# Kernel optimization log

Hardware: AMD Instinct MI355X
Metric: run time of the kernel (lower is better)

The kernel has to match this reference:

```python
import jax, jax.numpy as jnp
import numpy as np

# Model dims
H = 1024          # hidden_size
I = 2048          # intermediate_size
E = 8             # num_experts
IE = I // E       # expert_intermediate_size = 256
V = 100000        # vocab_size
B, S = 8, 2048


def _rowwise_quantize(x):
    """Dynamic per-row int8 quantization (faithful to dynamic_quantize_int8, per_channel=True).
    Returns quantized values kept in float32 (identical values to int8->float cast) and per-row scale."""
    max_vals = jnp.max(jnp.abs(x), axis=-1, keepdims=True)
    scale = jnp.maximum(max_vals / 127.0, 1e-8)
    x_q = jnp.clip(jnp.round(x / scale), -128.0, 127.0)
    return x_q, scale[..., 0]


def _quantize_weight(w):
    """Per-output-channel int8 quantization of a [K, N] weight (as in from_float)."""
    max_vals = jnp.max(jnp.abs(w), axis=0, keepdims=True)      # [1, N]
    scale = jnp.maximum(max_vals / 127.0, 1e-8)
    w_q = jnp.clip(jnp.round(w / scale), -128.0, 127.0).astype(jnp.int8)
    return w_q, scale[0]


def setup_inputs() -> dict:
    key = jax.random.key(0)
    ks = jax.random.split(key, 6)
    hidden_states = jax.random.normal(ks[0], (B, S, H), dtype=jnp.float32)
    token_ids = jax.random.randint(ks[1], (B, S), 0, V, dtype=jnp.int32)

    # Pre-quantized expert weights (int8) with per-output-channel fp32 scales.
    gate_w = jax.random.normal(ks[2], (E, H, IE), dtype=jnp.float32) * 0.02
    up_w = jax.random.normal(ks[3], (E, H, IE), dtype=jnp.float32) * 0.02
    down_w = jax.random.normal(ks[4], (E, IE, H), dtype=jnp.float32) * 0.02
    gate_q, gate_scale = jax.vmap(_quantize_weight)(gate_w)   # [E,H,IE] int8, [E,IE]
    up_q, up_scale = jax.vmap(_quantize_weight)(up_w)         # [E,H,IE] int8, [E,IE]
    down_q, down_scale = jax.vmap(_quantize_weight)(down_w)   # [E,IE,H] int8, [E,H]

    # Deterministic contiguous token->expert mapping (V divisible by E here).
    token_to_expert = jnp.minimum(jnp.arange(V, dtype=jnp.int32) // (V // E), E - 1)

    return {
        "hidden_states": hidden_states,
        "token_ids": token_ids,
        "gate_q": gate_q, "gate_scale": gate_scale,
        "up_q": up_q, "up_scale": up_scale,
        "down_q": down_q, "down_scale": down_scale,
        "token_to_expert": token_to_expert,
    }


def reference(hidden_states, token_ids, gate_q, gate_scale, up_q, up_scale,
              down_q, down_scale, token_to_expert):
    Bh, Sh, Hh = hidden_states.shape
    n_exp = gate_q.shape[0]
    vocab = token_to_expert.shape[0]

    tid = jnp.clip(token_ids, 0, vocab - 1)
    expert_ids = token_to_expert[tid].reshape(-1)             # [T]

    x = hidden_states.reshape(-1, Hh)                          # [T, H]
    # Per-row activation quantization is expert-independent -> do it once for all tokens.
    x_q, x_s = _rowwise_quantize(x)                            # [T,H], [T]

    gq = gate_q.astype(jnp.float32)
    uq = up_q.astype(jnp.float32)
    dq = down_q.astype(jnp.float32)

    out = jnp.zeros_like(x)
    for e in range(n_exp):  # small fixed expert count
        # fused quantize-GEMM: int8 matmul + per-row activation scale + per-col weight scale
        gate = (x_q @ gq[e]) * x_s[:, None] * gate_scale[e][None, :]   # [T, IE]
        up = (x_q @ uq[e]) * x_s[:, None] * up_scale[e][None, :]       # [T, IE]
        inter = jax.nn.silu(gate) * up
        i_q, i_s = _rowwise_quantize(inter)
        o = (i_q @ dq[e]) * i_s[:, None] * down_scale[e][None, :]      # [T, H]
        out = jnp.where((expert_ids == e)[:, None], o, out)
    return out.reshape(Bh, Sh, Hh)
```

## Files before the change

### kernel.cpp

```cpp
#include <hip/hip_runtime.h>

typedef int   int4v   __attribute__((ext_vector_type(4)));
typedef float float4v __attribute__((ext_vector_type(4)));

#define T_TOK 16384
#define HD    1024
#define IE    256
#define EN    8
#define VSZ   100000

#define M_OFF 16
#define M_TS1 25

#define XQ_OFF   0ull
#define PB1_OFF  21053440ull
#define PB2_OFF  25247744ull
#define PERM_OFF 27344896ull
#define XS_OFF   27410688ull
#define META_OFF 27542272ull
#define BC_OFF   27542528ull
#define BB_OFF   27544576ull

__device__ __forceinline__ void gload16(const void* g, void* l) {
    __builtin_amdgcn_global_load_lds(
        (const __attribute__((address_space(1))) unsigned int*)g,
        (__attribute__((address_space(3))) unsigned int*)l,
        16, 0, 0);
}

__global__ void k_hist(const int* __restrict__ ids, const int* __restrict__ t2e,
                       int* __restrict__ bc) {
    __shared__ int h[EN];
    if (threadIdx.x < EN) h[threadIdx.x] = 0;
    __syncthreads();
    int t = blockIdx.x * 256 + threadIdx.x;
    int id = ids[t]; id = min(max(id, 0), VSZ - 1);
    atomicAdd(&h[t2e[id]], 1);
    __syncthreads();
    if (threadIdx.x < EN) bc[blockIdx.x * EN + threadIdx.x] = h[threadIdx.x];
}

__global__ __launch_bounds__(512) void k_scan(const int* __restrict__ bc,
                                              int* __restrict__ bbase,
                                              int* __restrict__ meta) {
    int e = threadIdx.x >> 6;
    int b = threadIdx.x & 63;
    int c = bc[b * EN + e];
    int inc = c;
    #pragma unroll
    for (int s = 1; s < 64; s <<= 1) {
        int v = __shfl_up(inc, s, 64);
        if (b >= s) inc += v;
    }
    int exc = inc - c;
    __shared__ int tot[EN];
    __shared__ int goff[EN];
    if (b == 63) tot[e] = inc;
    __syncthreads();
    if (threadIdx.x == 0) {
        int off = 0, t1 = 0;
        meta[M_OFF] = 0; meta[M_TS1] = 0;
        #pragma unroll
        for (int i = 0; i < EN; ++i) {
            goff[i] = off;
            int cc = tot[i];
            off += cc; t1 += (cc + 31) >> 5;
            meta[M_OFF + i + 1] = off;
            meta[M_TS1 + i + 1] = t1;
        }
    }
    __syncthreads();
    bbase[b * EN + e] = goff[e] + exc;
}

__global__ void k_assign(const int* __restrict__ ids, const int* __restrict__ t2e,
                         const int* __restrict__ bbase, int* __restrict__ perm) {
    __shared__ int cur[EN];
    if (threadIdx.x < EN) cur[threadIdx.x] = bbase[blockIdx.x * EN + threadIdx.x];
    __syncthreads();
    int t = blockIdx.x * 256 + threadIdx.x;
    int id = ids[t]; id = min(max(id, 0), VSZ - 1);
    int e = t2e[id];
    int slot = atomicAdd(&cur[e], 1);
    perm[slot] = t;
}

__global__ __launch_bounds__(256) void k_pre(const float* __restrict__ hidden,
                                             const int* __restrict__ gq,
                                             const int* __restrict__ uq,
                                             const int* __restrict__ dq,
                                             signed char* __restrict__ xq,
                                             float* __restrict__ xs,
                                             signed char* __restrict__ pb1,
                                             signed char* __restrict__ pb2) {
    int b = blockIdx.x;
    if (b < 4096) {
        int w = threadIdx.x >> 6, lane = threadIdx.x & 63;
        int token = (b << 2) + w;
        const float* row = hidden + (size_t)token * HD;
        float v[16];
        #pragma unroll
        for (int j = 0; j < 4; ++j) {
            float4v f = *(const float4v*)(row + lane * 16 + j * 4);
            v[j*4+0] = f[0]; v[j*4+1] = f[1]; v[j*4+2] = f[2]; v[j*4+3] = f[3];
        }
        float mx = 0.0f;
        #pragma unroll
        for (int j = 0; j < 16; ++j) mx = fmaxf(mx, fabsf(v[j]));
        #pragma unroll
        for (int s = 1; s < 64; s <<= 1) mx = fmaxf(mx, __shfl_xor(mx, s, 64));
        float sc = fmaxf(mx / 127.0f, 1e-8f);
        if (lane == 0) xs[token] = sc;
        int4v pk;
        #pragma unroll
        for (int j = 0; j < 4; ++j) {
            int bb[4];
            #pragma unroll
            for (int u = 0; u < 4; ++u) {
                float t = rintf(v[j*4+u] / sc);
                t = fminf(fmaxf(t, -128.0f), 127.0f);
                bb[u] = (int)t;
            }
            pk[j] = (bb[0] & 255) | ((bb[1] & 255) << 8) | ((bb[2] & 255) << 16) | (bb[3] << 24);
        }
        *(int4v*)(xq + (size_t)token * HD + lane * 16) = pk;
    } else {
        int idx = (b - 4096) * 256 + threadIdx.x;
        if (idx < 262144) {
            int n = idx & 511, kc = (idx >> 9) & 63, e = idx >> 15;
            const int* src = (n < 256) ? gq + (((size_t)((e << 10) + (kc << 4)) << 8) + n)
                                       : uq + (((size_t)((e << 10) + (kc << 4)) << 8) + (n - 256));
            int4v pk;
            #pragma unroll
            for (int jj = 0; jj < 4; ++jj) {
                int b0 = src[(size_t)(jj * 4 + 0) << 8], b1 = src[(size_t)(jj * 4 + 1) << 8];
                int b2 = src[(size_t)(jj * 4 + 2) << 8], b3 = src[(size_t)(jj * 4 + 3) << 8];
                pk[jj] = (b0 & 255) | ((b1 & 255) << 8) | ((b2 & 255) << 16) | (b3 << 24);
            }
            *(int4v*)(pb1 + ((size_t)((((e << 6) + kc) << 9) + n) << 4)) = pk;
        } else {
            int j = idx - 262144;
            int n = j & 1023, kc = (j >> 10) & 15, e = j >> 14;
            const int* src = dq + (((size_t)((e << 8) + (kc << 4)) << 10) + n);
            int4v pk;
            #pragma unroll
            for (int jj = 0; jj < 4; ++jj) {
                int b0 = src[(size_t)(jj * 4 + 0) << 10], b1 = src[(size_t)(jj * 4 + 1) << 10];
                int b2 = src[(size_t)(jj * 4 + 2) << 10], b3 = src[(size_t)(jj * 4 + 3) << 10];
                pk[jj] = (b0 & 255) | ((b1 & 255) << 8) | ((b2 & 255) << 16) | (b3 << 24);
            }
            *(int4v*)(pb2 + ((size_t)((((e << 4) + kc) << 10) + n) << 4)) = pk;
        }
    }
}

__global__ __launch_bounds__(256, 2) void k_mlp(const signed char* __restrict__ xq,
                                                const signed char* __restrict__ pb1,
                                                const signed char* __restrict__ pb2,
                                                const float* __restrict__ xs,
                                                const float* __restrict__ gsc,
                                                const float* __restrict__ usc,
                                                const float* __restrict__ dsc,
                                                const int* __restrict__ meta,
                                                const int* __restrict__ perm,
                                                float* __restrict__ out) {
    int b = (blockIdx.x & 7) * 65 + (blockIdx.x >> 3);
    int e = -1, m0 = 0, gend = 0;
    #pragma unroll
    for (int i = 0; i < EN; ++i) {
        int s0 = meta[M_TS1 + i], s1 = meta[M_TS1 + i + 1];
        if (b >= s0 && b < s1) { e = i; m0 = meta[M_OFF + i] + ((b - s0) << 5); gend = meta[M_OFF + i + 1]; }
    }
    if (e < 0) return;
    const int w = threadIdx.x >> 6, lane = threadIdx.x & 63;
    const int q = lane >> 4, r = lane & 15;

    __shared__ __align__(16) signed char lB[2][32768];
    __shared__ __align__(16) signed char arena[8192];
    float* pmax = (float*)(arena + 4096);
    float* rsc  = (float*)(arena + 4608);
    int*   ptok = (int*)(arena + 4736);

    if (threadIdx.x < 32) ptok[threadIdx.x] = perm[min(m0 + (int)threadIdx.x, T_TOK - 1)];
    __syncthreads();

    int tokr[2][4];
    #pragma unroll
    for (int mi = 0; mi < 2; ++mi)
        #pragma unroll
        for (int g = 0; g < 4; ++g)
            tokr[mi][g] = ptok[(mi << 4) + (q << 2) + g];

    const signed char* pbe1 = pb1 + (size_t)e * (64 * 512 * 16);
    const signed char* pbe2 = pb2 + (size_t)e * (16 * 1024 * 16);
    const int arow = (w << 4) + (lane >> 2);
    const int acq  = (lane & 3) ^ ((lane >> 2) & 3);
    const signed char* ga_base = xq + (size_t)ptok[arow & 31] * HD + (acq << 4);

    #define G1_STAGE(buf, kt)                                                          \
        {                                                                              \
            int kc0 = (kt) << 2;                                                       \
            _Pragma("unroll")                                                          \
            for (int j = 0; j < 8; ++j) {                                              \
                int n = ((j << 6) + lane) ^ ((w & 1) << 3);                            \
                gload16(pbe1 + (((size_t)(kc0 + w) * 512 + n) << 4),                   \
                        &lB[buf][((w << 3) + j) << 10]);                               \
            }                                                                          \
            if (w < 2) gload16(ga_base + ((kt) << 6), arena + ((buf) << 11) + (w << 10)); \
        }

    #define G2_STAGE(buf, st)                                                          \
        {                                                                              \
            int kc0 = ((st) & 3) << 2; int nhs = (st) >> 2;                            \
            _Pragma("unroll")                                                          \
            for (int j = 0; j < 8; ++j) {                                              \
                int n = ((j << 6) + lane) ^ ((w & 1) << 3);                            \
                gload16(pbe2 + (((size_t)(kc0 + w) * 1024 + (nhs << 9) + n) << 4),     \
                        &lB[buf][((w << 3) + j) << 10]);                               \
            }                                                                          \
        }

    int4v zero = {0, 0, 0, 0};
    int4v accg[2][4], accu[2][4];
    #pragma unroll
    for (int mi = 0; mi < 2; ++mi)
        #pragma unroll
        for (int i = 0; i < 4; ++i) { accg[mi][i] = zero; accu[mi][i] = zero; }

    G1_STAGE(0, 0);
    for (int kt = 0; kt < 16; ++kt) {
        int cur = kt & 1;
        __syncthreads();
        if (kt < 15) G1_STAGE(cur ^ 1, kt + 1);
        int4v a[2];
        #pragma unroll
        for (int mi = 0; mi < 2; ++mi)
            a[mi] = *(const int4v*)&arena[(cur << 11) + ((((mi << 4) + r) << 6) + ((q ^ (r & 3)) << 4))];
        #pragma unroll
        for (int i = 0; i < 4; ++i) {
            int n = (w << 6) + (i << 4) + r;
            int sg = (q << 9) + (n ^ ((q & 1) << 3));
            int su = (q << 9) + ((n + 256) ^ ((q & 1) << 3));
            int4v bg = *(const int4v*)&lB[cur][sg << 4];
            int4v bu = *(const int4v*)&lB[cur][su << 4];
            #pragma unroll
            for (int mi = 0; mi < 2; ++mi) {
                accg[mi][i] = __builtin_amdgcn_mfma_i32_16x16x64_i8(a[mi], bg, accg[mi][i], 0, 0, 0);
                accu[mi][i] = __builtin_amdgcn_mfma_i32_16x16x64_i8(a[mi], bu, accu[mi][i], 0, 0, 0);
            }
        }
    }
    #undef G1_STAGE

    G2_STAGE(0, 0);

    float gs[4], us[4];
    #pragma unroll
    for (int i = 0; i < 4; ++i) {
        int n = (w << 6) + (i << 4) + r;
        gs[i] = gsc[e * IE + n];
        us[i] = usc[e * IE + n];
    }
    float xsr[2][4];
    #pragma unroll
    for (int mi = 0; mi < 2; ++mi)
        #pragma unroll
        for (int g = 0; g < 4; ++g)
            xsr[mi][g] = xs[tokr[mi][g]];

    float inter[2][4][4];
    float pm[2][4];
    #pragma unroll
    for (int mi = 0; mi < 2; ++mi)
        #pragma unroll
        for (int g = 0; g < 4; ++g) {
            float mx = 0.0f;
            #pragma unroll
            for (int i = 0; i < 4; ++i) {
                float gv = (float)accg[mi][i][g] * xsr[mi][g] * gs[i];
                float uv = (float)accu[mi][i][g] * xsr[mi][g] * us[i];
                float sg = gv / (1.0f + expf(-gv));
                float vv = sg * uv;
                inter[mi][i][g] = vv;
                mx = fmaxf(mx, fabsf(vv));
            }
            #pragma unroll
            for (int s = 1; s < 16; s <<= 1) mx = fmaxf(mx, __shfl_xor(mx, s, 64));
            pm[mi][g] = mx;
        }

    __syncthreads();
    if (r == 0) {
        #pragma unroll
        for (int mi = 0; mi < 2; ++mi)
            #pragma unroll
            for (int g = 0; g < 4; ++g)
                pmax[(w << 5) + (mi << 4) + (q << 2) + g] = pm[mi][g];
    }
    __syncthreads();
    if (threadIdx.x < 32) {
        int row = threadIdx.x;
        float mx = fmaxf(fmaxf(pmax[row], pmax[32 + row]), fmaxf(pmax[64 + row], pmax[96 + row]));
        rsc[row] = fmaxf(mx / 127.0f, 1e-8f);
    }
    __syncthreads();
    float rscr[2][4];
    #pragma unroll
    for (int mi = 0; mi < 2; ++mi)
        #pragma unroll
        for (int g = 0; g < 4; ++g)
            rscr[mi][g] = rsc[(mi << 4) + (q << 2) + g];
    __syncthreads();

    #pragma unroll
    for (int mi = 0; mi < 2; ++mi)
        #pragma unroll
        for (int g = 0; g < 4; ++g) {
            int row = (mi << 4) + (q << 2) + g;
            float sc = rscr[mi][g];
            #pragma unroll
            for (int i = 0; i < 4; ++i) {
                float t = rintf(inter[mi][i][g] / sc);
                t = fminf(fmaxf(t, -128.0f), 127.0f);
                arena[(row << 8) + ((((w << 2) + i) ^ (row & 3)) << 4) + r] = (signed char)(int)t;
            }
        }

    int4v acc2[2][8];
    for (int st = 0; st < 8; ++st) {
        int cur = st & 1;
        __syncthreads();
        if (st < 7) G2_STAGE(cur ^ 1, st + 1);
        if ((st & 3) == 0) {
            #pragma unroll
            for (int mi = 0; mi < 2; ++mi)
                #pragma unroll
                for (int i = 0; i < 8; ++i) acc2[mi][i] = zero;
        }
        int4v a2[2];
        #pragma unroll
        for (int mi = 0; mi < 2; ++mi) {
            int row2 = (mi << 4) + r;
            a2[mi] = *(const int4v*)&arena[(row2 << 8) + (((((st & 3) << 2) + q) ^ (r & 3)) << 4)];
        }
        #pragma unroll
        for (int i = 0; i < 8; ++i) {
            int n = (w << 7) + (i << 4) + r;
            int sb = (q << 9) + (n ^ ((q & 1) << 3));
            int4v bb = *(const int4v*)&lB[cur][sb << 4];
            #pragma unroll
            for (int mi = 0; mi < 2; ++mi)
                acc2[mi][i] = __builtin_amdgcn_mfma_i32_16x16x64_i8(a2[mi], bb, acc2[mi][i], 0, 0, 0);
        }
        if ((st & 3) == 3) {
            int nhs = st >> 2;
            float ds[8];
            #pragma unroll
            for (int i = 0; i < 8; ++i)
                ds[i] = dsc[e * HD + (nhs << 9) + (w << 7) + (i << 4) + r];
            #pragma unroll
            for (int mi = 0; mi < 2; ++mi)
                #pragma unroll
                for (int g = 0; g < 4; ++g) {
                    int slot = m0 + (mi << 4) + (q << 2) + g;
                    if (slot < gend) {
                        size_t ob = (size_t)tokr[mi][g] * HD + (nhs << 9) + (w << 7) + r;
                        #pragma unroll
                        for (int i = 0; i < 8; ++i)
                            out[ob + (i << 4)] = (float)acc2[mi][i][g] * rscr[mi][g] * ds[i];
                    }
                }
        }
    }
    #undef G2_STAGE
}

extern "C" void kernel_launch(void* const* d_in, const int* in_sizes, int n_in,
                              void* d_out, int out_size, void* d_ws, size_t ws_size,
                              hipStream_t stream) {
    const float* hidden = (const float*)d_in[0];
    const int*   ids    = (const int*)d_in[1];
    const int*   gq     = (const int*)d_in[2];
    const float* gsc    = (const float*)d_in[3];
    const int*   uq     = (const int*)d_in[4];
    const float* usc    = (const float*)d_in[5];
    const int*   dq     = (const int*)d_in[6];
    const float* dsc    = (const float*)d_in[7];
    const int*   t2e    = (const int*)d_in[8];
    float* out = (float*)d_out;

    char* ws = (char*)d_ws;
    signed char* xq  = (signed char*)(ws + XQ_OFF);
    signed char* pb1 = (signed char*)(ws + PB1_OFF);
    signed char* pb2 = (signed char*)(ws + PB2_OFF);
    int*   perm = (int*)(ws + PERM_OFF);
    float* xs   = (float*)(ws + XS_OFF);
    int*   meta = (int*)(ws + META_OFF);
    int*   bc   = (int*)(ws + BC_OFF);
    int*   bbase= (int*)(ws + BB_OFF);

    k_hist<<<64, 256, 0, stream>>>(ids, t2e, bc);
    k_scan<<<1, 512, 0, stream>>>(bc, bbase, meta);
    k_assign<<<64, 256, 0, stream>>>(ids, t2e, bbase, perm);
    k_pre<<<5632, 256, 0, stream>>>(hidden, gq, uq, dq, xq, xs, pb1, pb2);
    k_mlp<<<520, 256, 0, stream>>>(xq, pb1, pb2, xs, gsc, usc, dsc, meta, perm, out);
}
```

Before: 204.6 us.

## Double M tile to 64 tokens and triple-buffer LDS with cross-phase prefetch

```diff
diff --git a/kernel.cpp b/kernel.cpp
--- a/kernel.cpp
+++ b/kernel.cpp
@@ -28,6 +28,12 @@
         16, 0, 0);
 }
 
+#define LDS_BAR() do { \
+    asm volatile("s_waitcnt lgkmcnt(0)" ::: "memory"); \
+    __builtin_amdgcn_s_barrier(); \
+    __builtin_amdgcn_sched_barrier(0); \
+} while (0)
+
 __global__ void k_hist(const int* __restrict__ ids, const int* __restrict__ t2e,
                        int* __restrict__ bc) {
     __shared__ int h[EN];
@@ -64,7 +70,7 @@
         for (int i = 0; i < EN; ++i) {
             goff[i] = off;
             int cc = tot[i];
-            off += cc; t1 += (cc + 31) >> 5;
+            off += cc; t1 += (cc + 63) >> 6;
             meta[M_OFF + i + 1] = off;
             meta[M_TS1 + i + 1] = t1;
         }
@@ -154,7 +160,7 @@
     }
 }
 
-__global__ __launch_bounds__(256, 2) void k_mlp(const signed char* __restrict__ xq,
+__global__ __launch_bounds__(256, 1) void k_mlp(const signed char* __restrict__ xq,
                                                 const signed char* __restrict__ pb1,
                                                 const signed char* __restrict__ pb2,
                                                 const float* __restrict__ xs,
@@ -164,29 +170,29 @@
                                                 const int* __restrict__ meta,
                                                 const int* __restrict__ perm,
                                                 float* __restrict__ out) {
-    int b = (blockIdx.x & 7) * 65 + (blockIdx.x >> 3);
+    int b = (blockIdx.x & 7) * 33 + (blockIdx.x >> 3);
     int e = -1, m0 = 0, gend = 0;
     #pragma unroll
     for (int i = 0; i < EN; ++i) {
         int s0 = meta[M_TS1 + i], s1 = meta[M_TS1 + i + 1];
-        if (b >= s0 && b < s1) { e = i; m0 = meta[M_OFF + i] + ((b - s0) << 5); gend = meta[M_OFF + i + 1]; }
+        if (b >= s0 && b < s1) { e = i; m0 = meta[M_OFF + i] + ((b - s0) << 6); gend = meta[M_OFF + i + 1]; }
     }
     if (e < 0) return;
     const int w = threadIdx.x >> 6, lane = threadIdx.x & 63;
     const int q = lane >> 4, r = lane & 15;
 
-    __shared__ __align__(16) signed char lB[2][32768];
-    __shared__ __align__(16) signed char arena[8192];
-    float* pmax = (float*)(arena + 4096);
-    float* rsc  = (float*)(arena + 4608);
-    int*   ptok = (int*)(arena + 4736);
-
-    if (threadIdx.x < 32) ptok[threadIdx.x] = perm[min(m0 + (int)threadIdx.x, T_TOK - 1)];
-    __syncthreads();
-
-    int tokr[2][4];
-    #pragma unroll
-    for (int mi = 0; mi < 2; ++mi)
+    __shared__ __align__(16) signed char lB[3][32768];
+    __shared__ __align__(16) signed char arena[16384];
+    float* pmax = (float*)(arena + 12288);
+    float* rsc  = (float*)(arena + 13312);
+    int*   ptok = (int*)(arena + 13568);
+
+    if (threadIdx.x < 64) ptok[threadIdx.x] = perm[min(m0 + (int)threadIdx.x, T_TOK - 1)];
+    __syncthreads();
+
+    int tokr[4][4];
+    #pragma unroll
+    for (int mi = 0; mi < 4; ++mi)
         #pragma unroll
         for (int g = 0; g < 4; ++g)
             tokr[mi][g] = ptok[(mi << 4) + (q << 2) + g];
@@ -195,7 +201,27 @@
     const signed char* pbe2 = pb2 + (size_t)e * (16 * 1024 * 16);
     const int arow = (w << 4) + (lane >> 2);
     const int acq  = (lane & 3) ^ ((lane >> 2) & 3);
-    const signed char* ga_base = xq + (size_t)ptok[arow & 31] * HD + (acq << 4);
+    const signed char* ga_base = xq + (size_t)ptok[arow] * HD + (acq << 4);
+
+    float gs[4], us[4];
+    #pragma unroll
+    for (int i = 0; i < 4; ++i) {
+        int n = (w << 6) + (i << 4) + r;
+        gs[i] = gsc[e * IE + n];
+        us[i] = usc[e * IE + n];
+    }
+    float xsr[4][4];
+    #pragma unroll
+    for (int mi = 0; mi < 4; ++mi)
+        #pragma unroll
+        for (int g = 0; g < 4; ++g)
+            xsr[mi][g] = xs[tokr[mi][g]];
+    float ds16[2][8];
+    #pragma unroll
+    for (int nh = 0; nh < 2; ++nh)
+        #pragma unroll
+        for (int i = 0; i < 8; ++i)
+            ds16[nh][i] = dsc[e * HD + (nh << 9) + (w << 7) + (i << 4) + r];
 
     #define G1_STAGE(buf, kt)                                                          \
         {                                                                              \
@@ -206,12 +232,12 @@
                 gload16(pbe1 + (((size_t)(kc0 + w) * 512 + n) << 4),                   \
                         &lB[buf][((w << 3) + j) << 10]);                               \
             }                                                                          \
-            if (w < 2) gload16(ga_base + ((kt) << 6), arena + ((buf) << 11) + (w << 10)); \
-        }
-
-    #define G2_STAGE(buf, st)                                                          \
+            gload16(ga_base + ((kt) << 6), arena + ((buf) << 12) + (w << 10));         \
+        }
+
+    #define G2_STAGE(buf, st2)                                                         \
         {                                                                              \
-            int kc0 = ((st) & 3) << 2; int nhs = (st) >> 2;                            \
+            int kc0 = ((st2) & 3) << 2; int nhs = (st2) >> 2;                          \
             _Pragma("unroll")                                                          \
             for (int j = 0; j < 8; ++j) {                                              \
                 int n = ((j << 6) + lane) ^ ((w & 1) << 3);                            \
@@ -221,21 +247,28 @@
         }
 
     int4v zero = {0, 0, 0, 0};
-    int4v accg[2][4], accu[2][4];
-    #pragma unroll
-    for (int mi = 0; mi < 2; ++mi)
+    int4v accg[4][4], accu[4][4];
+    #pragma unroll
+    for (int mi = 0; mi < 4; ++mi)
         #pragma unroll
         for (int i = 0; i < 4; ++i) { accg[mi][i] = zero; accu[mi][i] = zero; }
 
     G1_STAGE(0, 0);
+    G1_STAGE(1, 1);
+
     for (int kt = 0; kt < 16; ++kt) {
-        int cur = kt & 1;
-        __syncthreads();
-        if (kt < 15) G1_STAGE(cur ^ 1, kt + 1);
-        int4v a[2];
-        #pragma unroll
-        for (int mi = 0; mi < 2; ++mi)
-            a[mi] = *(const int4v*)&arena[(cur << 11) + ((((mi << 4) + r) << 6) + ((q ^ (r & 3)) << 4))];
+        if (kt < 15) { asm volatile("s_waitcnt vmcnt(9) lgkmcnt(0)" ::: "memory"); }
+        else         { asm volatile("s_waitcnt vmcnt(8) lgkmcnt(0)" ::: "memory"); }
+        __builtin_amdgcn_s_barrier();
+        __builtin_amdgcn_sched_barrier(0);
+        int nxt = kt + 2;
+        if (nxt < 16)      { G1_STAGE(nxt % 3, nxt); }
+        else if (nxt < 18) { G2_STAGE(nxt % 3, nxt - 16); }
+        int cur = kt % 3;
+        int4v a[4];
+        #pragma unroll
+        for (int mi = 0; mi < 4; ++mi)
+            a[mi] = *(const int4v*)&arena[(cur << 12) + ((((mi << 4) + r) << 6) + ((q ^ (r & 3)) << 4))];
         #pragma unroll
         for (int i = 0; i < 4; ++i) {
             int n = (w << 6) + (i << 4) + r;
@@ -244,7 +277,7 @@
             int4v bg = *(const int4v*)&lB[cur][sg << 4];
             int4v bu = *(const int4v*)&lB[cur][su << 4];
             #pragma unroll
-            for (int mi = 0; mi < 2; ++mi) {
+            for (int mi = 0; mi < 4; ++mi) {
                 accg[mi][i] = __builtin_amdgcn_mfma_i32_16x16x64_i8(a[mi], bg, accg[mi][i], 0, 0, 0);
                 accu[mi][i] = __builtin_amdgcn_mfma_i32_16x16x64_i8(a[mi], bu, accu[mi][i], 0, 0, 0);
             }
@@ -252,26 +285,10 @@
     }
     #undef G1_STAGE
 
-    G2_STAGE(0, 0);
-
-    float gs[4], us[4];
-    #pragma unroll
-    for (int i = 0; i < 4; ++i) {
-        int n = (w << 6) + (i << 4) + r;
-        gs[i] = gsc[e * IE + n];
-        us[i] = usc[e * IE + n];
-    }
-    float xsr[2][4];
-    #pragma unroll
-    for (int mi = 0; mi < 2; ++mi)
-        #pragma unroll
-        for (int g = 0; g < 4; ++g)
-            xsr[mi][g] = xs[tokr[mi][g]];
-
-    float inter[2][4][4];
-    float pm[2][4];
-    #pragma unroll
-    for (int mi = 0; mi < 2; ++mi)
+    float inter[4][4][4];
+    float pm[4][4];
+    #pragma unroll
+    for (int mi = 0; mi < 4; ++mi)
         #pragma unroll
         for (int g = 0; g < 4; ++g) {
             float mx = 0.0f;
@@ -289,31 +306,30 @@
             pm[mi][g] = mx;
         }
 
-    __syncthreads();
     if (r == 0) {
         #pragma unroll
-        for (int mi = 0; mi < 2; ++mi)
+        for (int mi = 0; mi < 4; ++mi)
             #pragma unroll
             for (int g = 0; g < 4; ++g)
-                pmax[(w << 5) + (mi << 4) + (q << 2) + g] = pm[mi][g];
-    }
-    __syncthreads();
-    if (threadIdx.x < 32) {
+                pmax[(w << 6) + (mi << 4) + (q << 2) + g] = pm[mi][g];
+    }
+    LDS_BAR();
+    if (threadIdx.x < 64) {
         int row = threadIdx.x;
-        float mx = fmaxf(fmaxf(pmax[row], pmax[32 + row]), fmaxf(pmax[64 + row], pmax[96 + row]));
+        float mx = fmaxf(fmaxf(pmax[row], pmax[64 + row]), fmaxf(pmax[128 + row], pmax[192 + row]));
         rsc[row] = fmaxf(mx / 127.0f, 1e-8f);
     }
-    __syncthreads();
-    float rscr[2][4];
-    #pragma unroll
-    for (int mi = 0; mi < 2; ++mi)
+    LDS_BAR();
+    float rscr[4][4];
+    #pragma unroll
+    for (int mi = 0; mi < 4; ++mi)
         #pragma unroll
         for (int g = 0; g < 4; ++g)
             rscr[mi][g] = rsc[(mi << 4) + (q << 2) + g];
-    __syncthreads();
-
-    #pragma unroll
-    for (int mi = 0; mi < 2; ++mi)
+    LDS_BAR();
+
+    #pragma unroll
+    for (int mi = 0; mi < 4; ++mi)
         #pragma unroll
         for (int g = 0; g < 4; ++g) {
             int row = (mi << 4) + (q << 2) + g;
@@ -326,20 +342,23 @@
             }
         }
 
-    int4v acc2[2][8];
+    int4v acc2[4][8];
     for (int st = 0; st < 8; ++st) {
-        int cur = st & 1;
-        __syncthreads();
-        if (st < 7) G2_STAGE(cur ^ 1, st + 1);
+        if (st < 7) { asm volatile("s_waitcnt vmcnt(8) lgkmcnt(0)" ::: "memory"); }
+        else        { asm volatile("s_waitcnt vmcnt(0) lgkmcnt(0)" ::: "memory"); }
+        __builtin_amdgcn_s_barrier();
+        __builtin_amdgcn_sched_barrier(0);
+        if (st + 2 < 8) { G2_STAGE((18 + st) % 3, st + 2); }
         if ((st & 3) == 0) {
             #pragma unroll
-            for (int mi = 0; mi < 2; ++mi)
+            for (int mi = 0; mi < 4; ++mi)
                 #pragma unroll
                 for (int i = 0; i < 8; ++i) acc2[mi][i] = zero;
         }
-        int4v a2[2];
-        #pragma unroll
-        for (int mi = 0; mi < 2; ++mi) {
+        int cur = (16 + st) % 3;
+        int4v a2[4];
+        #pragma unroll
+        for (int mi = 0; mi < 4; ++mi) {
             int row2 = (mi << 4) + r;
             a2[mi] = *(const int4v*)&arena[(row2 << 8) + (((((st & 3) << 2) + q) ^ (r & 3)) << 4)];
         }
@@ -349,17 +368,13 @@
             int sb = (q << 9) + (n ^ ((q & 1) << 3));
             int4v bb = *(const int4v*)&lB[cur][sb << 4];
             #pragma unroll
-            for (int mi = 0; mi < 2; ++mi)
+            for (int mi = 0; mi < 4; ++mi)
                 acc2[mi][i] = __builtin_amdgcn_mfma_i32_16x16x64_i8(a2[mi], bb, acc2[mi][i], 0, 0, 0);
         }
         if ((st & 3) == 3) {
             int nhs = st >> 2;
-            float ds[8];
-            #pragma unroll
-            for (int i = 0; i < 8; ++i)
-                ds[i] = dsc[e * HD + (nhs << 9) + (w << 7) + (i << 4) + r];
-            #pragma unroll
-            for (int mi = 0; mi < 2; ++mi)
+            #pragma unroll
+            for (int mi = 0; mi < 4; ++mi)
                 #pragma unroll
                 for (int g = 0; g < 4; ++g) {
                     int slot = m0 + (mi << 4) + (q << 2) + g;
@@ -367,7 +382,7 @@
                         size_t ob = (size_t)tokr[mi][g] * HD + (nhs << 9) + (w << 7) + r;
                         #pragma unroll
                         for (int i = 0; i < 8; ++i)
-                            out[ob + (i << 4)] = (float)acc2[mi][i][g] * rscr[mi][g] * ds[i];
+                            out[ob + (i << 4)] = (float)acc2[mi][i][g] * rscr[mi][g] * ds16[nhs][i];
                     }
                 }
         }
@@ -403,5 +418,5 @@
     k_scan<<<1, 512, 0, stream>>>(bc, bbase, meta);
     k_assign<<<64, 256, 0, stream>>>(ids, t2e, bbase, perm);
     k_pre<<<5632, 256, 0, stream>>>(hidden, gq, uq, dq, xq, xs, pb1, pb2);
-    k_mlp<<<520, 256, 0, stream>>>(xq, pb1, pb2, xs, gsc, usc, dsc, meta, perm, out);
-}
+    k_mlp<<<264, 256, 0, stream>>>(xq, pb1, pb2, xs, gsc, usc, dsc, meta, perm, out);
+}
```

Result: slower. 230.0 us (+12.4%).

## Make MoE MLP kernel persistent with atomic tile queue and deeper prefetch

Applied to the files above, without the earlier changes.

```diff
diff --git a/kernel.cpp b/kernel.cpp
--- a/kernel.cpp
+++ b/kernel.cpp
@@ -20,6 +20,7 @@
 #define META_OFF 27542272ull
 #define BC_OFF   27542528ull
 #define BB_OFF   27544576ull
+#define TICK_OFF 27546624ull
 
 __device__ __forceinline__ void gload16(const void* g, void* l) {
     __builtin_amdgcn_global_load_lds(
@@ -28,10 +29,17 @@
         16, 0, 0);
 }
 
+#define LDS_BAR() do { \
+    asm volatile("s_waitcnt lgkmcnt(0)" ::: "memory"); \
+    __builtin_amdgcn_s_barrier(); \
+    __builtin_amdgcn_sched_barrier(0); \
+} while (0)
+
 __global__ void k_hist(const int* __restrict__ ids, const int* __restrict__ t2e,
-                       int* __restrict__ bc) {
+                       int* __restrict__ bc, int* __restrict__ tick) {
     __shared__ int h[EN];
     if (threadIdx.x < EN) h[threadIdx.x] = 0;
+    if (blockIdx.x == 0 && threadIdx.x == 0) tick[0] = 0;
     __syncthreads();
     int t = blockIdx.x * 256 + threadIdx.x;
     int id = ids[t]; id = min(max(id, 0), VSZ - 1);
@@ -163,216 +171,247 @@
                                                 const float* __restrict__ dsc,
                                                 const int* __restrict__ meta,
                                                 const int* __restrict__ perm,
+                                                int* tick,
                                                 float* __restrict__ out) {
-    int b = (blockIdx.x & 7) * 65 + (blockIdx.x >> 3);
-    int e = -1, m0 = 0, gend = 0;
-    #pragma unroll
-    for (int i = 0; i < EN; ++i) {
-        int s0 = meta[M_TS1 + i], s1 = meta[M_TS1 + i + 1];
-        if (b >= s0 && b < s1) { e = i; m0 = meta[M_OFF + i] + ((b - s0) << 5); gend = meta[M_OFF + i + 1]; }
-    }
-    if (e < 0) return;
     const int w = threadIdx.x >> 6, lane = threadIdx.x & 63;
     const int q = lane >> 4, r = lane & 15;
 
     __shared__ __align__(16) signed char lB[2][32768];
-    __shared__ __align__(16) signed char arena[8192];
-    float* pmax = (float*)(arena + 4096);
-    float* rsc  = (float*)(arena + 4608);
-    int*   ptok = (int*)(arena + 4736);
-
-    if (threadIdx.x < 32) ptok[threadIdx.x] = perm[min(m0 + (int)threadIdx.x, T_TOK - 1)];
-    __syncthreads();
-
-    int tokr[2][4];
+    __shared__ __align__(16) signed char iqt[8192];
+    __shared__ float pmax[128];
+    __shared__ float rsc[32];
+    __shared__ int   ptok[32];
+    __shared__ int   s_tile;
+
+    int mts[9], moff[9];
     #pragma unroll
-    for (int mi = 0; mi < 2; ++mi)
-        #pragma unroll
-        for (int g = 0; g < 4; ++g)
-            tokr[mi][g] = ptok[(mi << 4) + (q << 2) + g];
-
-    const signed char* pbe1 = pb1 + (size_t)e * (64 * 512 * 16);
-    const signed char* pbe2 = pb2 + (size_t)e * (16 * 1024 * 16);
-    const int arow = (w << 4) + (lane >> 2);
-    const int acq  = (lane & 3) ^ ((lane >> 2) & 3);
-    const signed char* ga_base = xq + (size_t)ptok[arow & 31] * HD + (acq << 4);
-
-    #define G1_STAGE(buf, kt)                                                          \
-        {                                                                              \
-            int kc0 = (kt) << 2;                                                       \
-            _Pragma("unroll")                                                          \
-            for (int j = 0; j < 8; ++j) {                                              \
-                int n = ((j << 6) + lane) ^ ((w & 1) << 3);                            \
-                gload16(pbe1 + (((size_t)(kc0 + w) * 512 + n) << 4),                   \
-                        &lB[buf][((w << 3) + j) << 10]);                               \
-            }                                                                          \
-            if (w < 2) gload16(ga_base + ((kt) << 6), arena + ((buf) << 11) + (w << 10)); \
-        }
-
-    #define G2_STAGE(buf, st)                                                          \
-        {                                                                              \
-            int kc0 = ((st) & 3) << 2; int nhs = (st) >> 2;                            \
-            _Pragma("unroll")                                                          \
-            for (int j = 0; j < 8; ++j) {                                              \
-                int n = ((j << 6) + lane) ^ ((w & 1) << 3);                            \
-                gload16(pbe2 + (((size_t)(kc0 + w) * 1024 + (nhs << 9) + n) << 4),     \
-                        &lB[buf][((w << 3) + j) << 10]);                               \
-            }                                                                          \
-        }
-
-    int4v zero = {0, 0, 0, 0};
-    int4v accg[2][4], accu[2][4];
-    #pragma unroll
-    for (int mi = 0; mi < 2; ++mi)
-        #pragma unroll
-        for (int i = 0; i < 4; ++i) { accg[mi][i] = zero; accu[mi][i] = zero; }
-
-    G1_STAGE(0, 0);
-    for (int kt = 0; kt < 16; ++kt) {
-        int cur = kt & 1;
+    for (int i = 0; i < 9; ++i) { mts[i] = meta[M_TS1 + i]; moff[i] = meta[M_OFF + i]; }
+    const int nt = mts[8];
+
+    for (;;) {
+        if (threadIdx.x == 0) s_tile = atomicAdd(tick, 1);
         __syncthreads();
-        if (kt < 15) G1_STAGE(cur ^ 1, kt + 1);
-        int4v a[2];
-        #pragma unroll
-        for (int mi = 0; mi < 2; ++mi)
-            a[mi] = *(const int4v*)&arena[(cur << 11) + ((((mi << 4) + r) << 6) + ((q ^ (r & 3)) << 4))];
+        int tile = s_tile;
+        if (tile >= nt) break;
+
+        int e = 0;
+        #pragma unroll
+        for (int i = 1; i < 8; ++i) if (tile >= mts[i]) e = i;
+        int m0 = moff[e] + ((tile - mts[e]) << 5);
+        int gend = moff[e + 1];
+
+        if (threadIdx.x < 32) ptok[threadIdx.x] = perm[min(m0 + (int)threadIdx.x, T_TOK - 1)];
+        __syncthreads();
+
+        int tokr[2][4];
+        #pragma unroll
+        for (int mi = 0; mi < 2; ++mi)
+            #pragma unroll
+            for (int g = 0; g < 4; ++g)
+                tokr[mi][g] = ptok[(mi << 4) + (q << 2) + g];
+        const signed char* aptr0 = xq + (size_t)ptok[r] * HD + (q << 4);
+        const signed char* aptr1 = xq + (size_t)ptok[16 + r] * HD + (q << 4);
+
+        const signed char* pbe1 = pb1 + (size_t)e * (64 * 512 * 16);
+        const signed char* pbe2 = pb2 + (size_t)e * (16 * 1024 * 16);
+
+        float gs[4], us[4];
         #pragma unroll
         for (int i = 0; i < 4; ++i) {
             int n = (w << 6) + (i << 4) + r;
-            int sg = (q << 9) + (n ^ ((q & 1) << 3));
-            int su = (q << 9) + ((n + 256) ^ ((q & 1) << 3));
-            int4v bg = *(const int4v*)&lB[cur][sg << 4];
-            int4v bu = *(const int4v*)&lB[cur][su << 4];
+            gs[i] = gsc[e * IE + n];
+            us[i] = usc[e * IE + n];
+        }
+        float xsr[2][4];
+        #pragma unroll
+        for (int mi = 0; mi < 2; ++mi)
+            #pragma unroll
+            for (int g = 0; g < 4; ++g)
+                xsr[mi][g] = xs[tokr[mi][g]];
+        float ds16[2][8];
+        #pragma unroll
+        for (int nh = 0; nh < 2; ++nh)
+            #pragma unroll
+            for (int i = 0; i < 8; ++i)
+                ds16[nh][i] = dsc[e * HD + (nh << 9) + (w << 7) + (i << 4) + r];
+
+        #define G1B(buf, kt)                                                           \
+            {                                                                          \
+                int kc0 = (kt) << 2;                                                   \
+                _Pragma("unroll")                                                      \
+                for (int j = 0; j < 8; ++j) {                                          \
+                    int n = ((j << 6) + lane) ^ ((w & 1) << 3);                        \
+                    gload16(pbe1 + (((size_t)(kc0 + w) * 512 + n) << 4),               \
+                            &lB[buf][((w << 3) + j) << 10]);                           \
+                }                                                                      \
+            }
+        #define G2B(buf, st2)                                                          \
+            {                                                                          \
+                int kc0 = ((st2) & 3) << 2; int nhs = (st2) >> 2;                      \
+                _Pragma("unroll")                                                      \
+                for (int j = 0; j < 8; ++j) {                                          \
+                    int n = ((j << 6) + lane) ^ ((w & 1) << 3);                        \
+                    gload16(pbe2 + (((size_t)(kc0 + w) * 1024 + (nhs << 9) + n) << 4), \
+                            &lB[buf][((w << 3) + j) << 10]);                           \
+                }                                                                      \
+            }
+
+        int4v zero = {0, 0, 0, 0};
+        int4v accg[2][4], accu[2][4];
+        #pragma unroll
+        for (int mi = 0; mi < 2; ++mi)
+            #pragma unroll
+            for (int i = 0; i < 4; ++i) { accg[mi][i] = zero; accu[mi][i] = zero; }
+
+        int4v areg[2][2];
+        G1B(0, 0);
+        areg[0][0] = *(const int4v*)(aptr0);
+        areg[0][1] = *(const int4v*)(aptr1);
+        G1B(1, 1);
+        areg[1][0] = *(const int4v*)(aptr0 + 64);
+        areg[1][1] = *(const int4v*)(aptr1 + 64);
+
+        #pragma unroll
+        for (int kt = 0; kt < 16; ++kt) {
+            if (kt < 15) { asm volatile("s_waitcnt vmcnt(10) lgkmcnt(0)" ::: "memory"); }
+            else         { asm volatile("s_waitcnt vmcnt(8) lgkmcnt(0)" ::: "memory"); }
+            __builtin_amdgcn_sched_barrier(0);
+            __builtin_amdgcn_s_barrier();
+            __builtin_amdgcn_sched_barrier(0);
+            const int cur = kt & 1;
+            int4v a0 = areg[cur][0], a1 = areg[cur][1];
+            #pragma unroll
+            for (int i = 0; i < 4; ++i) {
+                int n = (w << 6) + (i << 4) + r;
+                int sg = (q << 9) + (n ^ ((q & 1) << 3));
+                int su = (q << 9) + ((n + 256) ^ ((q & 1) << 3));
+                int4v bg = *(const int4v*)&lB[cur][sg << 4];
+                int4v bu = *(const int4v*)&lB[cur][su << 4];
+                accg[0][i] = __builtin_amdgcn_mfma_i32_16x16x64_i8(a0, bg, accg[0][i], 0, 0, 0);
+                accg[1][i] = __builtin_amdgcn_mfma_i32_16x16x64_i8(a1, bg, accg[1][i], 0, 0, 0);
+                accu[0][i] = __builtin_amdgcn_mfma_i32_16x16x64_i8(a0, bu, accu[0][i], 0, 0, 0);
+                accu[1][i] = __builtin_amdgcn_mfma_i32_16x16x64_i8(a1, bu, accu[1][i], 0, 0, 0);
+            }
+            __builtin_amdgcn_s_barrier();
+            __builtin_amdgcn_sched_barrier(0);
+            if (kt < 14) {
+                G1B(cur, kt + 2);
+                areg[cur][0] = *(const int4v*)(aptr0 + ((kt + 2) << 6));
+                areg[cur][1] = *(const int4v*)(aptr1 + ((kt + 2) << 6));
+            } else if (kt == 14) { G2B(0, 0); }
+            else                 { G2B(1, 1); }
+        }
+        #undef G1B
+
+        float inter[2][4][4];
+        float pm[2][4];
+        #pragma unroll
+        for (int mi = 0; mi < 2; ++mi)
+            #pragma unroll
+            for (int g = 0; g < 4; ++g) {
+                float mx = 0.0f;
+                #pragma unroll
+                for (int i = 0; i < 4; ++i) {
+                    float gv = (float)accg[mi][i][g] * xsr[mi][g] * gs[i];
+                    float uv = (float)accu[mi][i][g] * xsr[mi][g] * us[i];
+                    float sg = gv / (1.0f + expf(-gv));
+                    float vv = sg * uv;
+                    inter[mi][i][g] = vv;
+                    mx = fmaxf(mx, fabsf(vv));
+                }
+                #pragma unroll
+                for (int s = 1; s < 16; s <<= 1) mx = fmaxf(mx, __shfl_xor(mx, s, 64));
+                pm[mi][g] = mx;
+            }
+
+        if (r == 0) {
+            #pragma unroll
+            for (int mi = 0; mi < 2; ++mi)
+                #pragma unroll
+                for (int g = 0; g < 4; ++g)
+                    pmax[(w << 5) + (mi << 4) + (q << 2) + g] = pm[mi][g];
+        }
+        LDS_BAR();
+        if (threadIdx.x < 32) {
+            int row = threadIdx.x;
+            float mx = fmaxf(fmaxf(pmax[row], pmax[32 + row]), fmaxf(pmax[64 + row], pmax[96 + row]));
+            rsc[row] = fmaxf(mx / 127.0f, 1e-8f);
+        }
+        LDS_BAR();
+        float rscr[2][4];
+        #pragma unroll
+        for (int mi = 0; mi < 2; ++mi)
+            #pragma unroll
+            for (int g = 0; g < 4; ++g)
+                rscr[mi][g] = rsc[(mi << 4) + (q << 2) + g];
+
+        #pragma unroll
+        for (int mi = 0; mi < 2; ++mi)
+            #pragma unroll
+            for (int g = 0; g < 4; ++g) {
+                int row = (mi << 4) + (q << 2) + g;
+                float sc = rscr[mi][g];
+                #pragma unroll
+                for (int i = 0; i < 4; ++i) {
+                    float t = rintf(inter[mi][i][g] / sc);
+                    t = fminf(fmaxf(t, -128.0f), 127.0f);
+                    iqt[(row << 8) + ((((w << 2) + i) ^ (row & 3)) << 4) + r] = (signed char)(int)t;
+                }
+            }
+        LDS_BAR();
+
+        int4v acc2[2][8];
+        #pragma unroll
+        for (int st = 0; st < 8; ++st) {
+            if (st < 7) { asm volatile("s_waitcnt vmcnt(8) lgkmcnt(0)" ::: "memory"); }
+            else        { asm volatile("s_waitcnt vmcnt(0) lgkmcnt(0)" ::: "memory"); }
+            __builtin_amdgcn_sched_barrier(0);
+            __builtin_amdgcn_s_barrier();
+            __builtin_amdgcn_sched_barrier(0);
+            if ((st & 3) == 0) {
+                #pragma unroll
+                for (int mi = 0; mi < 2; ++mi)
+                    #pragma unroll
+                    for (int i = 0; i < 8; ++i) acc2[mi][i] = zero;
+            }
+            const int cur = st & 1;
+            int4v a2[2];
             #pragma unroll
             for (int mi = 0; mi < 2; ++mi) {
-                accg[mi][i] = __builtin_amdgcn_mfma_i32_16x16x64_i8(a[mi], bg, accg[mi][i], 0, 0, 0);
-                accu[mi][i] = __builtin_amdgcn_mfma_i32_16x16x64_i8(a[mi], bu, accu[mi][i], 0, 0, 0);
-            }
-        }
+                int row2 = (mi << 4) + r;
+                a2[mi] = *(const int4v*)&iqt[(row2 << 8) + (((((st & 3) << 2) + q) ^ (r & 3)) << 4)];
+            }
+            #pragma unroll
+            for (int i = 0; i < 8; ++i) {
+                int n = (w << 7) + (i << 4) + r;
+                int sb = (q << 9) + (n ^ ((q & 1) << 3));
+                int4v bb = *(const int4v*)&lB[cur][sb << 4];
+                acc2[0][i] = __builtin_amdgcn_mfma_i32_16x16x64_i8(a2[0], bb, acc2[0][i], 0, 0, 0);
+                acc2[1][i] = __builtin_amdgcn_mfma_i32_16x16x64_i8(a2[1], bb, acc2[1][i], 0, 0, 0);
+            }
+            if ((st & 3) == 3) {
+                int nhs = st >> 2;
+                #pragma unroll
+                for (int mi = 0; mi < 2; ++mi)
+                    #pragma unroll
+                    for (int g = 0; g < 4; ++g) {
+                        int slot = m0 + (mi << 4) + (q << 2) + g;
+                        if (slot < gend) {
+                            size_t ob = (size_t)tokr[mi][g] * HD + (nhs << 9) + (w << 7) + r;
+                            #pragma unroll
+                            for (int i = 0; i < 8; ++i)
+                                out[ob + (i << 4)] = (float)acc2[mi][i][g] * rscr[mi][g] * ds16[nhs][i];
+                        }
+                    }
+            }
+            __builtin_amdgcn_s_barrier();
+            __builtin_amdgcn_sched_barrier(0);
+            if (st < 6) { G2B(cur, st + 2); }
+        }
+        #undef G2B
+
+        __syncthreads();
     }
-    #undef G1_STAGE
-
-    G2_STAGE(0, 0);
-
-    float gs[4], us[4];
-    #pragma unroll
-    for (int i = 0; i < 4; ++i) {
-        int n = (w << 6) + (i << 4) + r;
-        gs[i] = gsc[e * IE + n];
-        us[i] = usc[e * IE + n];
-    }
-    float xsr[2][4];
-    #pragma unroll
-    for (int mi = 0; mi < 2; ++mi)
-        #pragma unroll
-        for (int g = 0; g < 4; ++g)
-            xsr[mi][g] = xs[tokr[mi][g]];
-
-    float inter[2][4][4];
-    float pm[2][4];
-    #pragma unroll
-    for (int mi = 0; mi < 2; ++mi)
-        #pragma unroll
-        for (int g = 0; g < 4; ++g) {
-            float mx = 0.0f;
-            #pragma unroll
-            for (int i = 0; i < 4; ++i) {
-                float gv = (float)accg[mi][i][g] * xsr[mi][g] * gs[i];
-                float uv = (float)accu[mi][i][g] * xsr[mi][g] * us[i];
-                float sg = gv / (1.0f + expf(-gv));
-                float vv = sg * uv;
-                inter[mi][i][g] = vv;
-                mx = fmaxf(mx, fabsf(vv));
-            }
-            #pragma unroll
-            for (int s = 1; s < 16; s <<= 1) mx = fmaxf(mx, __shfl_xor(mx, s, 64));
-            pm[mi][g] = mx;
-        }
-
-    __syncthreads();
-    if (r == 0) {
-        #pragma unroll
-        for (int mi = 0; mi < 2; ++mi)
-            #pragma unroll
-            for (int g = 0; g < 4; ++g)
-                pmax[(w << 5) + (mi << 4) + (q << 2) + g] = pm[mi][g];
-    }
-    __syncthreads();
-    if (threadIdx.x < 32) {
-        int row = threadIdx.x;
-        float mx = fmaxf(fmaxf(pmax[row], pmax[32 + row]), fmaxf(pmax[64 + row], pmax[96 + row]));
-        rsc[row] = fmaxf(mx / 127.0f, 1e-8f);
-    }
-    __syncthreads();
-    float rscr[2][4];
-    #pragma unroll
-    for (int mi = 0; mi < 2; ++mi)
-        #pragma unroll
-        for (int g = 0; g < 4; ++g)
-            rscr[mi][g] = rsc[(mi << 4) + (q << 2) + g];
-    __syncthreads();
-
-    #pragma unroll
-    for (int mi = 0; mi < 2; ++mi)
-        #pragma unroll
-        for (int g = 0; g < 4; ++g) {
-            int row = (mi << 4) + (q << 2) + g;
-            float sc = rscr[mi][g];
-            #pragma unroll
-            for (int i = 0; i < 4; ++i) {
-                float t = rintf(inter[mi][i][g] / sc);
-                t = fminf(fmaxf(t, -128.0f), 127.0f);
-                arena[(row << 8) + ((((w << 2) + i) ^ (row & 3)) << 4) + r] = (signed char)(int)t;
-            }
-        }
-
-    int4v acc2[2][8];
-    for (int st = 0; st < 8; ++st) {
-        int cur = st & 1;
-        __syncthreads();
-        if (st < 7) G2_STAGE(cur ^ 1, st + 1);
-        if ((st & 3) == 0) {
-            #pragma unroll
-            for (int mi = 0; mi < 2; ++mi)
-                #pragma unroll
-                for (int i = 0; i < 8; ++i) acc2[mi][i] = zero;
-        }
-        int4v a2[2];
-        #pragma unroll
-        for (int mi = 0; mi < 2; ++mi) {
-            int row2 = (mi << 4) + r;
-            a2[mi] = *(const int4v*)&arena[(row2 << 8) + (((((st & 3) << 2) + q) ^ (r & 3)) << 4)];
-        }
-        #pragma unroll
-        for (int i = 0; i < 8; ++i) {
-            int n = (w << 7) + (i << 4) + r;
-            int sb = (q << 9) + (n ^ ((q & 1) << 3));
-            int4v bb = *(const int4v*)&lB[cur][sb << 4];
-            #pragma unroll
-            for (int mi = 0; mi < 2; ++mi)
-                acc2[mi][i] = __builtin_amdgcn_mfma_i32_16x16x64_i8(a2[mi], bb, acc2[mi][i], 0, 0, 0);
-        }
-        if ((st & 3) == 3) {
-            int nhs = st >> 2;
-            float ds[8];
-            #pragma unroll
-            for (int i = 0; i < 8; ++i)
-                ds[i] = dsc[e * HD + (nhs << 9) + (w << 7) + (i << 4) + r];
-            #pragma unroll
-            for (int mi = 0; mi < 2; ++mi)
-                #pragma unroll
-                for (int g = 0; g < 4; ++g) {
-                    int slot = m0 + (mi << 4) + (q << 2) + g;
-                    if (slot < gend) {
-                        size_t ob = (size_t)tokr[mi][g] * HD + (nhs << 9) + (w << 7) + r;
-                        #pragma unroll
-                        for (int i = 0; i < 8; ++i)
-                            out[ob + (i << 4)] = (float)acc2[mi][i][g] * rscr[mi][g] * ds[i];
-                    }
-                }
-        }
-    }
-    #undef G2_STAGE
 }
 
 extern "C" void kernel_launch(void* const* d_in, const int* in_sizes, int n_in,
@@ -398,10 +437,11 @@
     int*   meta = (int*)(ws + META_OFF);
     int*   bc   = (int*)(ws + BC_OFF);
     int*   bbase= (int*)(ws + BB_OFF);
-
-    k_hist<<<64, 256, 0, stream>>>(ids, t2e, bc);
+    int*   tick = (int*)(ws + TICK_OFF);
+
+    k_hist<<<64, 256, 0, stream>>>(ids, t2e, bc, tick);
     k_scan<<<1, 512, 0, stream>>>(bc, bbase, meta);
     k_assign<<<64, 256, 0, stream>>>(ids, t2e, bbase, perm);
     k_pre<<<5632, 256, 0, stream>>>(hidden, gq, uq, dq, xq, xs, pb1, pb2);
-    k_mlp<<<520, 256, 0, stream>>>(xq, pb1, pb2, xs, gsc, usc, dsc, meta, perm, out);
-}
+    k_mlp<<<512, 256, 0, stream>>>(xq, pb1, pb2, xs, gsc, usc, dsc, meta, perm, tick, out);
+}
```

New measurement: 363.3 us. 77.6% more time.
